# Optimization experiments

Measured on AMD Instinct MI355X. Metric: run time of the kernel, lower is better.

Reference implementation:

```python
import jax, jax.numpy as jnp
import numpy as np

B, N, C, H, R, E = 64, 512, 64, 8, 17, 21
HD = C // H
BETA = 0.01


def setup_inputs() -> dict:
    key = jax.random.key(0)
    ks = jax.random.split(key, 13)
    s = 0.02
    x = jax.random.normal(ks[0], (B, N, C), jnp.float32)
    ext = jax.random.normal(ks[1], (B, N, E), jnp.float32)
    # soft sector-assignment tensor (dense float, as used by the einsum)
    assignment = jax.random.uniform(ks[2], (N, N, R), jnp.float32)
    mask = jax.random.randint(ks[3], (N, R), 0, 2) == 1
    mask = mask.at[:, 0].set(False)  # guarantee >=1 unmasked sector per node
    Wq = jax.random.normal(ks[4], (C, C), jnp.float32) * s
    Wkv = jax.random.normal(ks[5], (2 * C, C), jnp.float32) * s
    relative_bias = jax.random.normal(ks[6], (H, 1, R), jnp.float32)
    W1 = jax.random.normal(ks[7], (64, E), jnp.float32) * s
    b1 = jnp.zeros((64,), jnp.float32)
    W2 = jax.random.normal(ks[8], (H * R, 64), jnp.float32) * s
    b2 = jnp.zeros((H * R,), jnp.float32)
    Wp = jax.random.normal(ks[9], (C, C), jnp.float32) * s
    bp = jnp.zeros((C,), jnp.float32)
    return dict(x=x, ext=ext, assignment=assignment, Wq=Wq, Wkv=Wkv,
                relative_bias=relative_bias, W1=W1, b1=b1, W2=W2, b2=b2,
                Wp=Wp, bp=bp, mask=mask)


def reference(x, ext, assignment, Wq, Wkv, relative_bias, W1, b1, W2, b2, Wp, bp, mask):
    scale = HD ** (-0.5)
    # sector gather: [B,N,C] x [N,N,R] -> [B,N,R,C]
    pre_kv = jnp.einsum('bnc,mnr->bmrc', x, assignment)
    # projections (torch Linear: y = x @ W^T)
    q = (x @ Wq.T).reshape(B, N, H, HD)                 # per-token single query
    kv = pre_kv @ Wkv.T                                  # [B,N,R,2C]
    k, v = jnp.split(kv, 2, axis=-1)
    k = k.reshape(B, N, R, H, HD)
    v = v.reshape(B, N, R, H, HD)
    # tiny 1xR attention per (b,n,h)
    attn = jnp.einsum('bnhd,bnrhd->bnhr', q, k) * scale
    attn = attn + relative_bias[:, 0, :][None, None]     # [H,R] broadcast
    # ext modulation
    ext_imp = jax.nn.relu(ext @ W1.T + b1) @ W2.T + b2   # [B,N,H*R] (dropout=eval)
    attn = attn + BETA * ext_imp.reshape(B, N, H, R)
    attn = jnp.where(mask[None, :, None, :], -jnp.inf, attn)
    p = jax.nn.softmax(attn, axis=-1)
    out = jnp.einsum('bnhr,bnrhd->bnhd', p, v).reshape(B, N, C)
    return out @ Wp.T + bp
```

## Files before the change

kernel.cpp:

```cpp
#include <hip/hip_runtime.h>
#include <hip/hip_bf16.h>

typedef __bf16 bf16x8 __attribute__((ext_vector_type(8)));
typedef float f32x4 __attribute__((ext_vector_type(4)));

#define NN 512
#define NR 17

__device__ __forceinline__ __bf16 f2b(float f) {
  __hip_bfloat16 h = __float2bfloat16(f);
  return __builtin_bit_cast(__bf16, h);
}

__device__ __forceinline__ void gload_lds16(const void* g, void* l) {
  __builtin_amdgcn_global_load_lds(
      (const __attribute__((address_space(1))) void*)g,
      (__attribute__((address_space(3))) void*)l, 16, 0, 0);
}

__global__ __launch_bounds__(256) void pack_A(const float* __restrict__ a,
                                              __hip_bfloat16* __restrict__ A2) {
  __shared__ __hip_bfloat16 T[NR * 136];
  const int m = blockIdx.y;
  const int n0 = blockIdx.x * 128;
  const float* src = a + (size_t)m * (NN * NR) + (size_t)n0 * NR;
  for (int t = threadIdx.x; t < 128 * NR; t += 256) {
    int i = t / NR;
    int r = t - i * NR;
    T[r * 136 + i] = __float2bfloat16(src[t]);
  }
  __syncthreads();
  for (int t = threadIdx.x; t < NR * 128; t += 256) {
    int r = t >> 7;
    int i = t & 127;
    A2[((size_t)m * NR + r) * NN + n0 + i] = T[r * 136 + i];
  }
}

__global__ __launch_bounds__(256) void pack_X(const float* __restrict__ x,
                                              __hip_bfloat16* __restrict__ XT,
                                              __hip_bfloat16* __restrict__ XR, int b0) {
  __shared__ __hip_bfloat16 T[64 * 136];
  const int by = blockIdx.y;
  const int n0 = blockIdx.x * 128;
  const float* src = x + ((size_t)(b0 + by) * NN + n0) * 64;
  for (int t = threadIdx.x; t < 128 * 64; t += 256) {
    int i = t >> 6;
    int c = t & 63;
    __hip_bfloat16 v = __float2bfloat16(src[t]);
    T[c * 136 + i] = v;
    XR[((size_t)by * NN + n0 + i) * 64 + c] = v;
  }
  __syncthreads();
  for (int t = threadIdx.x; t < 64 * 128; t += 256) {
    int c = t >> 7;
    int i = t & 127;
    XT[((size_t)by * 64 + c) * NN + n0 + i] = T[c * 136 + i];
  }
}

__global__ __launch_bounds__(256) void prep_w(const float* __restrict__ Wq,
                                              const float* __restrict__ Wkv,
                                              const float* __restrict__ Wp,
                                              __hip_bfloat16* __restrict__ WQK,
                                              __hip_bfloat16* __restrict__ WVP) {
  const int base = blockIdx.x * 512 + threadIdx.x;
#pragma unroll
  for (int k = 0; k < 2; ++k) {
    const int idx = base + k * 256;
    {
      const int i = idx & 63, row = idx >> 6, h = row >> 6, c = row & 63;
      float a = 0.f;
#pragma unroll
      for (int d = 0; d < 8; ++d) a += Wq[(h * 8 + d) * 64 + i] * Wkv[(h * 8 + d) * 64 + c];
      WQK[idx] = __float2bfloat16(a * 0.35355339059327373f);
    }
    {
      const int hc = idx & 511, j = idx >> 9, h = hc >> 6, c = hc & 63;
      float a = 0.f;
#pragma unroll
      for (int d = 0; d < 8; ++d)
        a += Wkv[4096 + (h * 8 + d) * 64 + c] * Wp[j * 64 + (h * 8 + d)];
      WVP[idx] = __float2bfloat16(a);
    }
  }
}

__global__ __launch_bounds__(256) void gemm_prekv(const __hip_bfloat16* __restrict__ A2,
                                                  const __hip_bfloat16* __restrict__ XT,
                                                  __hip_bfloat16* __restrict__ pkv) {
  __shared__ char As[16384];
  __shared__ char Bs[16384];
  const int tid = threadIdx.x;
  const int wave = tid >> 6;
  const int lane = tid & 63;
  const int rowBase = blockIdx.y * 128;
  const int colBase = blockIdx.x * 128;
  const int wrow0 = (wave >> 1) * 64;
  const int wcol0 = (wave & 1) * 64;
  const int lrow8 = lane >> 3;
  const int gslot = lane & 7;
  const int gsrc = gslot ^ lrow8;

  f32x4 acc[4][4];
#pragma unroll
  for (int i = 0; i < 4; ++i)
#pragma unroll
    for (int j = 0; j < 4; ++j) acc[i][j] = (f32x4)0.0f;

  const int fr = lane & 15;
  const int kg = lane >> 4;

  for (int kt = 0; kt < NN; kt += 64) {
#pragma unroll
    for (int cc = 0; cc < 4; ++cc) {
      const int r0 = wave * 32 + cc * 8;
      gload_lds16(A2 + ((size_t)(rowBase + r0 + lrow8) * NN + kt + gsrc * 8), As + r0 * 128);
      gload_lds16(XT + ((size_t)(colBase + r0 + lrow8) * NN + kt + gsrc * 8), Bs + r0 * 128);
    }
    __syncthreads();
#pragma unroll
    for (int kk = 0; kk < 2; ++kk) {
      bf16x8 av[4], bv[4];
#pragma unroll
      for (int mi = 0; mi < 4; ++mi) {
        const int row = wrow0 + mi * 16 + fr;
        const int slot = (kk * 4 + kg) ^ (row & 7);
        av[mi] = *(const bf16x8*)(As + row * 128 + slot * 16);
      }
#pragma unroll
      for (int ni = 0; ni < 4; ++ni) {
        const int row = wcol0 + ni * 16 + fr;
        const int slot = (kk * 4 + kg) ^ (row & 7);
        bv[ni] = *(const bf16x8*)(Bs + row * 128 + slot * 16);
      }
#pragma unroll
      for (int mi = 0; mi < 4; ++mi)
#pragma unroll
        for (int ni = 0; ni < 4; ++ni)
          acc[mi][ni] =
              __builtin_amdgcn_mfma_f32_16x16x32_bf16(av[mi], bv[ni], acc[mi][ni], 0, 0, 0);
    }
    __syncthreads();
  }

  const int rq = lane >> 4;
#pragma unroll
  for (int mi = 0; mi < 4; ++mi) {
#pragma unroll
    for (int ni = 0; ni < 4; ++ni) {
#pragma unroll
      for (int reg = 0; reg < 4; ++reg) {
        const int gi = rowBase + wrow0 + mi * 16 + rq * 4 + reg;
        const int gj = colBase + wcol0 + ni * 16 + fr;
        const unsigned m = (unsigned)gi / 17u;
        const unsigned r = (unsigned)gi - m * 17u;
        const int bb = gj >> 6;
        const int c = gj & 63;
        pkv[(((size_t)bb * NN + m) * NR + r) * 64 + c] = __float2bfloat16(acc[mi][ni][reg]);
      }
    }
  }
}

__global__ __launch_bounds__(256) void qw_gemm(const __hip_bfloat16* __restrict__ XR,
                                               const __hip_bfloat16* __restrict__ WQK,
                                               __hip_bfloat16* __restrict__ QW) {
  __shared__ char As[16384];
  __shared__ char Bs[16384];
  const int tid = threadIdx.x;
  const int wave = tid >> 6;
  const int lane = tid & 63;
  const int rowBase = blockIdx.y * 128;
  const int colBase = blockIdx.x * 128;
  const int wrow0 = (wave >> 1) * 64;
  const int wcol0 = (wave & 1) * 64;
  const int lrow8 = lane >> 3;
  const int gslot = lane & 7;
  const int gsrc = gslot ^ lrow8;
  const int fr = lane & 15;
  const int kg = lane >> 4;

  f32x4 acc[4][4];
#pragma unroll
  for (int i = 0; i < 4; ++i)
#pragma unroll
    for (int j = 0; j < 4; ++j) acc[i][j] = (f32x4)0.0f;

#pragma unroll
  for (int cc = 0; cc < 4; ++cc) {
    const int r0 = wave * 32 + cc * 8;
    gload_lds16(XR + ((size_t)(rowBase + r0 + lrow8) * 64 + gsrc * 8), As + r0 * 128);
    gload_lds16(WQK + ((size_t)(colBase + r0 + lrow8) * 64 + gsrc * 8), Bs + r0 * 128);
  }
  __syncthreads();
#pragma unroll
  for (int kk = 0; kk < 2; ++kk) {
    bf16x8 av[4], bv[4];
#pragma unroll
    for (int mi = 0; mi < 4; ++mi) {
      const int row = wrow0 + mi * 16 + fr;
      const int slot = (kk * 4 + kg) ^ (row & 7);
      av[mi] = *(const bf16x8*)(As + row * 128 + slot * 16);
    }
#pragma unroll
    for (int ni = 0; ni < 4; ++ni) {
      const int row = wcol0 + ni * 16 + fr;
      const int slot = (kk * 4 + kg) ^ (row & 7);
      bv[ni] = *(const bf16x8*)(Bs + row * 128 + slot * 16);
    }
#pragma unroll
    for (int mi = 0; mi < 4; ++mi)
#pragma unroll
      for (int ni = 0; ni < 4; ++ni)
        acc[mi][ni] =
            __builtin_amdgcn_mfma_f32_16x16x32_bf16(av[mi], bv[ni], acc[mi][ni], 0, 0, 0);
  }

  const int rq = lane >> 4;
#pragma unroll
  for (int mi = 0; mi < 4; ++mi)
#pragma unroll
    for (int ni = 0; ni < 4; ++ni)
#pragma unroll
      for (int reg = 0; reg < 4; ++reg) {
        const int gi = rowBase + wrow0 + mi * 16 + rq * 4 + reg;
        const int gj = colBase + wcol0 + ni * 16 + fr;
        QW[(size_t)gi * 512 + gj] = __float2bfloat16(acc[mi][ni][reg]);
      }
}

__global__ __launch_bounds__(256) void ei_kernel(const float* __restrict__ ext,
                                                 const float* __restrict__ W1p,
                                                 const float* __restrict__ b1p,
                                                 const float* __restrict__ W2p,
                                                 const float* __restrict__ b2p,
                                                 const float* __restrict__ rbp,
                                                 const int* __restrict__ maskp,
                                                 float* __restrict__ EIF, int ct0) {
  __shared__ float exts[64 * 21];
  __shared__ float W1s[64 * 21];
  __shared__ __hip_bfloat16 Hl[64 * 72];
  const int tid = threadIdx.x;
  const int tblk = blockIdx.x * 64;
  for (int i = tid; i < 64 * 21; i += 256) {
    exts[i] = ext[(size_t)(ct0 + tblk) * 21 + i];
    W1s[i] = W1p[i];
  }
  __syncthreads();
  const int wave = tid >> 6, lane = tid & 63;
#pragma unroll
  for (int k = 0; k < 16; ++k) {
    const int tl = k * 4 + wave;
    float a = b1p[lane];
#pragma unroll
    for (int e = 0; e < 21; ++e) a += exts[tl * 21 + e] * W1s[lane * 21 + e];
    Hl[tl * 72 + lane] = __float2bfloat16(fmaxf(a, 0.f));
  }
  __syncthreads();
  const int fr = lane & 15, kg = lane >> 4;
  const __bf16* Hb = (const __bf16*)Hl;
  bf16x8 a0 = *(const bf16x8*)(Hb + (wave * 16 + fr) * 72 + kg * 8);
  bf16x8 a1 = *(const bf16x8*)(Hb + (wave * 16 + fr) * 72 + 32 + kg * 8);
#pragma unroll
  for (int tile = 0; tile < 9; ++tile) {
    const int o = tile * 16 + fr;
    bf16x8 bv0 = (bf16x8)f2b(0.0f), bv1 = (bf16x8)f2b(0.0f);
    if (o < 136) {
#pragma unroll
      for (int jj = 0; jj < 8; ++jj) {
        bv0[jj] = f2b(W2p[o * 64 + kg * 8 + jj]);
        bv1[jj] = f2b(W2p[o * 64 + 32 + kg * 8 + jj]);
      }
    }
    f32x4 acc = (f32x4)0.0f;
    acc = __builtin_amdgcn_mfma_f32_16x16x32_bf16(a0, bv0, acc, 0, 0, 0);
    acc = __builtin_amdgcn_mfma_f32_16x16x32_bf16(a1, bv1, acc, 0, 0, 0);
    if (o < 136) {
      const int h = (o * 241) >> 12;
      const int r = o - h * 17;
      const float rbo = rbp[o], b2o = b2p[o];
#pragma unroll
      for (int reg = 0; reg < 4; ++reg) {
        const int tl = tblk + wave * 16 + kg * 4 + reg;
        const int m = (ct0 + tl) & (NN - 1);
        float v = maskp[m * NR + r] ? -1e30f : (rbo + 0.01f * (acc[reg] + b2o));
        EIF[(size_t)tl * 136 + o] = v;
      }
    }
  }
}

__global__ __launch_bounds__(256) void attn_fused(const __hip_bfloat16* __restrict__ pkvB,
                                                  const __hip_bfloat16* __restrict__ qwB,
                                                  const float* __restrict__ eifB,
                                                  __hip_bfloat16* __restrict__ tB) {
  __shared__ __hip_bfloat16 ps[4][16 * 40];
  const int tid = threadIdx.x;
  const int wave = tid >> 6;
  const int lane = tid & 63;
  const int t = blockIdx.x * 4 + wave;
  const __bf16* qw = (const __bf16*)(qwB + (size_t)t * 512);
  const __bf16* pkv = (const __bf16*)(pkvB + (size_t)t * (NR * 64));
  const float* eif = eifB + (size_t)t * 136;
  const int fr = lane & 15;
  const int kg = lane >> 4;

  f32x4 slo = (f32x4)0.0f, shi = (f32x4)0.0f;
#pragma unroll
  for (int kk = 0; kk < 2; ++kk) {
    bf16x8 av = *(const bf16x8*)(qw + fr * 64 + kk * 32 + kg * 8);
    bf16x8 blo = *(const bf16x8*)(pkv + fr * 64 + kk * 32 + kg * 8);
    bf16x8 bhi = (bf16x8)f2b(0.0f);
    if (fr == 0) bhi = *(const bf16x8*)(pkv + 16 * 64 + kk * 32 + kg * 8);
    slo = __builtin_amdgcn_mfma_f32_16x16x32_bf16(av, blo, slo, 0, 0, 0);
    shi = __builtin_amdgcn_mfma_f32_16x16x32_bf16(av, bhi, shi, 0, 0, 0);
  }

  float plo[4], phi[4];
#pragma unroll
  for (int reg = 0; reg < 4; ++reg) {
    const int h = kg * 4 + reg;
    float llo = slo[reg] + eif[h * 17 + fr];
    float lhi = (fr == 0) ? (shi[reg] + eif[h * 17 + 16]) : -1e30f;
    float mx = fmaxf(llo, lhi);
    mx = fmaxf(mx, __shfl_xor(mx, 1));
    mx = fmaxf(mx, __shfl_xor(mx, 2));
    mx = fmaxf(mx, __shfl_xor(mx, 4));
    mx = fmaxf(mx, __shfl_xor(mx, 8));
    float el = __expf(llo - mx);
    float eh = __expf(lhi - mx);
    float sm = el + eh;
    sm += __shfl_xor(sm, 1);
    sm += __shfl_xor(sm, 2);
    sm += __shfl_xor(sm, 4);
    sm += __shfl_xor(sm, 8);
    const float iv = 1.0f / sm;
    plo[reg] = el * iv;
    phi[reg] = eh * iv;
  }

  __hip_bfloat16* pw = ps[wave];
#pragma unroll
  for (int reg = 0; reg < 4; ++reg) {
    const int h = kg * 4 + reg;
    pw[h * 40 + fr] = __float2bfloat16(plo[reg]);
    pw[h * 40 + 16 + fr] = __float2bfloat16(phi[reg]);
  }
  bf16x8 ap = *(const bf16x8*)((const __bf16*)pw + fr * 40 + kg * 8);

#pragma unroll
  for (int ni = 0; ni < 4; ++ni) {
    bf16x8 bv = (bf16x8)f2b(0.0f);
    const __bf16* bsrc = pkv + ni * 16 + fr;
#pragma unroll
    for (int jj = 0; jj < 8; ++jj) {
      const int r = kg * 8 + jj;
      if (r < NR) bv[jj] = bsrc[r * 64];
    }
    f32x4 o = __builtin_amdgcn_mfma_f32_16x16x32_bf16(ap, bv, (f32x4)0.0f, 0, 0, 0);
    if (kg < 2) {
#pragma unroll
      for (int reg = 0; reg < 4; ++reg) {
        const int h = kg * 4 + reg;
        tB[(size_t)t * 512 + h * 64 + ni * 16 + fr] = __float2bfloat16(o[reg]);
      }
    }
  }
}

__global__ __launch_bounds__(256) void out_gemm(const __hip_bfloat16* __restrict__ Tb,
                                                const __hip_bfloat16* __restrict__ WVP,
                                                const float* __restrict__ bp,
                                                float* __restrict__ out, int ct0) {
  __shared__ char As[16384];
  __shared__ char Bs[8192];
  const int tid = threadIdx.x;
  const int wave = tid >> 6;
  const int lane = tid & 63;
  const int rowBase = blockIdx.x * 128;
  const int lrow8 = lane >> 3;
  const int gslot = lane & 7;
  const int gsrc = gslot ^ lrow8;
  const int fr = lane & 15;
  const int kg = lane >> 4;

  f32x4 acc[2][4];
#pragma unroll
  for (int i = 0; i < 2; ++i)
#pragma unroll
    for (int j = 0; j < 4; ++j) acc[i][j] = (f32x4)0.0f;

  for (int kt = 0; kt < 8; ++kt) {
#pragma unroll
    for (int cc = 0; cc < 4; ++cc) {
      const int r0 = wave * 32 + cc * 8;
      gload_lds16(Tb + ((size_t)(rowBase + r0 + lrow8) * 512 + kt * 64 + gsrc * 8),
                  As + r0 * 128);
    }
#pragma unroll
    for (int cc = 0; cc < 2; ++cc) {
      const int r0 = cc * 32 + wave * 8;
      gload_lds16(WVP + ((size_t)(r0 + lrow8) * 512 + kt * 64 + gsrc * 8), Bs + r0 * 128);
    }
    __syncthreads();
#pragma unroll
    for (int kk = 0; kk < 2; ++kk) {
      bf16x8 av[2], bv[4];
#pragma unroll
      for (int mi = 0; mi < 2; ++mi) {
        const int row = wave * 32 + mi * 16 + fr;
        const int slot = (kk * 4 + kg) ^ (row & 7);
        av[mi] = *(const bf16x8*)(As + row * 128 + slot * 16);
      }
#pragma unroll
      for (int ni = 0; ni < 4; ++ni) {
        const int row = ni * 16 + fr;
        const int slot = (kk * 4 + kg) ^ (row & 7);
        bv[ni] = *(const bf16x8*)(Bs + row * 128 + slot * 16);
      }
#pragma unroll
      for (int mi = 0; mi < 2; ++mi)
#pragma unroll
        for (int ni = 0; ni < 4; ++ni)
          acc[mi][ni] =
              __builtin_amdgcn_mfma_f32_16x16x32_bf16(av[mi], bv[ni], acc[mi][ni], 0, 0, 0);
    }
    __syncthreads();
  }

  const int rq = lane >> 4;
#pragma unroll
  for (int mi = 0; mi < 2; ++mi)
#pragma unroll
    for (int ni = 0; ni < 4; ++ni) {
      const int gj = ni * 16 + fr;
      const float bpv = bp[gj];
#pragma unroll
      for (int reg = 0; reg < 4; ++reg) {
        const int gi = rowBase + wave * 32 + mi * 16 + rq * 4 + reg;
        out[(size_t)(ct0 + gi) * 64 + gj] = acc[mi][ni][reg] + bpv;
      }
    }
}

extern "C" void kernel_launch(void* const* d_in, const int* in_sizes, int n_in, void* d_out,
                              int out_size, void* d_ws, size_t ws_size, hipStream_t stream) {
  const float* x = (const float*)d_in[0];
  const float* ext = (const float*)d_in[1];
  const float* assign = (const float*)d_in[2];
  const float* Wq = (const float*)d_in[3];
  const float* Wkv = (const float*)d_in[4];
  const float* rb = (const float*)d_in[5];
  const float* W1 = (const float*)d_in[6];
  const float* b1 = (const float*)d_in[7];
  const float* W2 = (const float*)d_in[8];
  const float* b2 = (const float*)d_in[9];
  const float* Wp = (const float*)d_in[10];
  const float* bp = (const float*)d_in[11];
  const int* mask = (const int*)d_in[12];
  float* out = (float*)d_out;

  char* ws = (char*)d_ws;
  const size_t szA2 = 8912896;
  const size_t szWQK = 65536;
  const size_t szWVP = 65536;
  const size_t fixed = szA2 + szWQK + szWVP;

  int nchunks = 4;
  {
    const int cand[3] = {1, 2, 4};
    for (int ci = 0; ci < 3; ++ci) {
      const size_t ntk = 32768 / cand[ci];
      const size_t nbb = 64 / cand[ci];
      const size_t need = fixed + nbb * 65536 + ntk * 128 + ntk * 2176 +
                          (ntk * 1024 + 2048) + (ntk * 544 + 4096) + ntk * 1024;
      if (need <= ws_size) { nchunks = cand[ci]; break; }
    }
  }
  const int ntok = 32768 / nchunks;
  const int nb = 64 / nchunks;

  __hip_bfloat16* A2 = (__hip_bfloat16*)(ws);
  __hip_bfloat16* WQK = (__hip_bfloat16*)(ws + szA2);
  __hip_bfloat16* WVP = (__hip_bfloat16*)(ws + szA2 + szWQK);
  char* p = ws + fixed;
  __hip_bfloat16* XT = (__hip_bfloat16*)p;
  p += (size_t)nb * 65536;
  __hip_bfloat16* XR = (__hip_bfloat16*)p;
  p += (size_t)ntok * 128;
  __hip_bfloat16* PKV = (__hip_bfloat16*)p;
  p += (size_t)ntok * 2176;
  __hip_bfloat16* QW = (__hip_bfloat16*)p;
  p += (size_t)ntok * 1024 + 2048;
  float* EIF = (float*)p;
  p += (size_t)ntok * 544 + 4096;
  __hip_bfloat16* TBUF = (__hip_bfloat16*)p;

  hipLaunchKernelGGL(pack_A, dim3(4, 512), dim3(256), 0, stream, assign, A2);
  hipLaunchKernelGGL(prep_w, dim3(64), dim3(256), 0, stream, Wq, Wkv, Wp, WQK, WVP);

  for (int ck = 0; ck < nchunks; ++ck) {
    const int b0 = ck * nb;
    const int ct0 = ck * ntok;
    hipLaunchKernelGGL(pack_X, dim3(4, nb), dim3(256), 0, stream, x, XT, XR, b0);
    hipLaunchKernelGGL(gemm_prekv, dim3(nb / 2, 68), dim3(256), 0, stream, A2, XT, PKV);
    hipLaunchKernelGGL(qw_gemm, dim3(4, ntok / 128), dim3(256), 0, stream, XR, WQK, QW);
    hipLaunchKernelGGL(ei_kernel, dim3(ntok / 64), dim3(256), 0, stream, ext, W1, b1, W2, b2,
                       rb, mask, EIF, ct0);
    hipLaunchKernelGGL(attn_fused, dim3(ntok / 4), dim3(256), 0, stream, PKV, QW, EIF, TBUF);
    hipLaunchKernelGGL(out_gemm, dim3(ntok / 128), dim3(256), 0, stream, TBUF, WVP, bp, out,
                       ct0);
  }
}
```

Measured before the change: 269.2 us.

## Fuse QW gemm, attention and output projection into one mega kernel; drop chunking

Replaces the separate qw_gemm, attn_fused and out_gemm kernels with a single attn_mega kernel that computes the per-token query projection into LDS, runs the 1xR attention, and applies the output projection from LDS. This removes the QW and TBUF global round trips. The per-chunk loop goes away in favour of a single full-size launch with fixed workspace offsets, and gemm_prekv gets a block-index remap for better cache locality. Risks include heavy LDS use (80KB dynamic) limiting occupancy, and an early return if the workspace is too small.

```diff
diff --git a/kernel.cpp b/kernel.cpp
--- a/kernel.cpp
+++ b/kernel.cpp
@@ -6,6 +6,8 @@
 
 #define NN 512
 #define NR 17
+
+#define SWZ(row, b) (((((b) >> 4) ^ ((row) & 7)) << 4) | ((b) & 15))
 
 __device__ __forceinline__ __bf16 f2b(float f) {
   __hip_bfloat16 h = __float2bfloat16(f);
@@ -39,11 +41,11 @@
 
 __global__ __launch_bounds__(256) void pack_X(const float* __restrict__ x,
                                               __hip_bfloat16* __restrict__ XT,
-                                              __hip_bfloat16* __restrict__ XR, int b0) {
+                                              __hip_bfloat16* __restrict__ XR) {
   __shared__ __hip_bfloat16 T[64 * 136];
   const int by = blockIdx.y;
   const int n0 = blockIdx.x * 128;
-  const float* src = x + ((size_t)(b0 + by) * NN + n0) * 64;
+  const float* src = x + ((size_t)by * NN + n0) * 64;
   for (int t = threadIdx.x; t < 128 * 64; t += 256) {
     int i = t >> 6;
     int c = t & 63;
@@ -86,6 +88,7 @@
   }
 }
 
+#define PREKV_NWG 2176
 __global__ __launch_bounds__(256) void gemm_prekv(const __hip_bfloat16* __restrict__ A2,
                                                   const __hip_bfloat16* __restrict__ XT,
                                                   __hip_bfloat16* __restrict__ pkv) {
@@ -94,8 +97,10 @@
   const int tid = threadIdx.x;
   const int wave = tid >> 6;
   const int lane = tid & 63;
-  const int rowBase = blockIdx.y * 128;
-  const int colBase = blockIdx.x * 128;
+  const int flat = blockIdx.y * gridDim.x + blockIdx.x;
+  const int s = (flat & 7) * (PREKV_NWG / 8) + (flat >> 3);
+  const int rowBase = (s >> 5) * 128;
+  const int colBase = (s & 31) * 128;
   const int wrow0 = (wave >> 1) * 64;
   const int wcol0 = (wave & 1) * 64;
   const int lrow8 = lane >> 3;
@@ -163,73 +168,6 @@
   }
 }
 
-__global__ __launch_bounds__(256) void qw_gemm(const __hip_bfloat16* __restrict__ XR,
-                                               const __hip_bfloat16* __restrict__ WQK,
-                                               __hip_bfloat16* __restrict__ QW) {
-  __shared__ char As[16384];
-  __shared__ char Bs[16384];
-  const int tid = threadIdx.x;
-  const int wave = tid >> 6;
-  const int lane = tid & 63;
-  const int rowBase = blockIdx.y * 128;
-  const int colBase = blockIdx.x * 128;
-  const int wrow0 = (wave >> 1) * 64;
-  const int wcol0 = (wave & 1) * 64;
-  const int lrow8 = lane >> 3;
-  const int gslot = lane & 7;
-  const int gsrc = gslot ^ lrow8;
-  const int fr = lane & 15;
-  const int kg = lane >> 4;
-
-  f32x4 acc[4][4];
-#pragma unroll
-  for (int i = 0; i < 4; ++i)
-#pragma unroll
-    for (int j = 0; j < 4; ++j) acc[i][j] = (f32x4)0.0f;
-
-#pragma unroll
-  for (int cc = 0; cc < 4; ++cc) {
-    const int r0 = wave * 32 + cc * 8;
-    gload_lds16(XR + ((size_t)(rowBase + r0 + lrow8) * 64 + gsrc * 8), As + r0 * 128);
-    gload_lds16(WQK + ((size_t)(colBase + r0 + lrow8) * 64 + gsrc * 8), Bs + r0 * 128);
-  }
-  __syncthreads();
-#pragma unroll
-  for (int kk = 0; kk < 2; ++kk) {
-    bf16x8 av[4], bv[4];
-#pragma unroll
-    for (int mi = 0; mi < 4; ++mi) {
-      const int row = wrow0 + mi * 16 + fr;
-      const int slot = (kk * 4 + kg) ^ (row & 7);
-      av[mi] = *(const bf16x8*)(As + row * 128 + slot * 16);
-    }
-#pragma unroll
-    for (int ni = 0; ni < 4; ++ni) {
-      const int row = wcol0 + ni * 16 + fr;
-      const int slot = (kk * 4 + kg) ^ (row & 7);
-      bv[ni] = *(const bf16x8*)(Bs + row * 128 + slot * 16);
-    }
-#pragma unroll
-    for (int mi = 0; mi < 4; ++mi)
-#pragma unroll
-      for (int ni = 0; ni < 4; ++ni)
-        acc[mi][ni] =
-            __builtin_amdgcn_mfma_f32_16x16x32_bf16(av[mi], bv[ni], acc[mi][ni], 0, 0, 0);
-  }
-
-  const int rq = lane >> 4;
-#pragma unroll
-  for (int mi = 0; mi < 4; ++mi)
-#pragma unroll
-    for (int ni = 0; ni < 4; ++ni)
-#pragma unroll
-      for (int reg = 0; reg < 4; ++reg) {
-        const int gi = rowBase + wrow0 + mi * 16 + rq * 4 + reg;
-        const int gj = colBase + wcol0 + ni * 16 + fr;
-        QW[(size_t)gi * 512 + gj] = __float2bfloat16(acc[mi][ni][reg]);
-      }
-}
-
 __global__ __launch_bounds__(256) void ei_kernel(const float* __restrict__ ext,
                                                  const float* __restrict__ W1p,
                                                  const float* __restrict__ b1p,
@@ -237,14 +175,14 @@
                                                  const float* __restrict__ b2p,
                                                  const float* __restrict__ rbp,
                                                  const int* __restrict__ maskp,
-                                                 float* __restrict__ EIF, int ct0) {
+                                                 float* __restrict__ EIF) {
   __shared__ float exts[64 * 21];
   __shared__ float W1s[64 * 21];
   __shared__ __hip_bfloat16 Hl[64 * 72];
   const int tid = threadIdx.x;
   const int tblk = blockIdx.x * 64;
   for (int i = tid; i < 64 * 21; i += 256) {
-    exts[i] = ext[(size_t)(ct0 + tblk) * 21 + i];
+    exts[i] = ext[(size_t)tblk * 21 + i];
     W1s[i] = W1p[i];
   }
   __syncthreads();
@@ -283,7 +221,7 @@
 #pragma unroll
       for (int reg = 0; reg < 4; ++reg) {
         const int tl = tblk + wave * 16 + kg * 4 + reg;
-        const int m = (ct0 + tl) & (NN - 1);
+        const int m = tl & (NN - 1);
         float v = maskp[m * NR + r] ? -1e30f : (rbo + 0.01f * (acc[reg] + b2o));
         EIF[(size_t)tl * 136 + o] = v;
       }
@@ -291,157 +229,160 @@
   }
 }
 
-__global__ __launch_bounds__(256) void attn_fused(const __hip_bfloat16* __restrict__ pkvB,
-                                                  const __hip_bfloat16* __restrict__ qwB,
-                                                  const float* __restrict__ eifB,
-                                                  __hip_bfloat16* __restrict__ tB) {
-  __shared__ __hip_bfloat16 ps[4][16 * 40];
+__global__ __launch_bounds__(256, 2) void attn_mega(
+    const __hip_bfloat16* __restrict__ XRp, const __hip_bfloat16* __restrict__ WQKp,
+    const __hip_bfloat16* __restrict__ WVPp, const __hip_bfloat16* __restrict__ pkvB,
+    const float* __restrict__ eifB, const float* __restrict__ bpp,
+    float* __restrict__ outp) {
+  extern __shared__ char smem[];
+  char* qws = smem;
+  char* Ts = smem + 32768;
   const int tid = threadIdx.x;
   const int wave = tid >> 6;
   const int lane = tid & 63;
-  const int t = blockIdx.x * 4 + wave;
-  const __bf16* qw = (const __bf16*)(qwB + (size_t)t * 512);
-  const __bf16* pkv = (const __bf16*)(pkvB + (size_t)t * (NR * 64));
-  const float* eif = eifB + (size_t)t * 136;
   const int fr = lane & 15;
   const int kg = lane >> 4;
-
-  f32x4 slo = (f32x4)0.0f, shi = (f32x4)0.0f;
-#pragma unroll
-  for (int kk = 0; kk < 2; ++kk) {
-    bf16x8 av = *(const bf16x8*)(qw + fr * 64 + kk * 32 + kg * 8);
-    bf16x8 blo = *(const bf16x8*)(pkv + fr * 64 + kk * 32 + kg * 8);
-    bf16x8 bhi = (bf16x8)f2b(0.0f);
-    if (fr == 0) bhi = *(const bf16x8*)(pkv + 16 * 64 + kk * 32 + kg * 8);
-    slo = __builtin_amdgcn_mfma_f32_16x16x32_bf16(av, blo, slo, 0, 0, 0);
-    shi = __builtin_amdgcn_mfma_f32_16x16x32_bf16(av, bhi, shi, 0, 0, 0);
-  }
-
-  float plo[4], phi[4];
-#pragma unroll
-  for (int reg = 0; reg < 4; ++reg) {
-    const int h = kg * 4 + reg;
-    float llo = slo[reg] + eif[h * 17 + fr];
-    float lhi = (fr == 0) ? (shi[reg] + eif[h * 17 + 16]) : -1e30f;
-    float mx = fmaxf(llo, lhi);
-    mx = fmaxf(mx, __shfl_xor(mx, 1));
-    mx = fmaxf(mx, __shfl_xor(mx, 2));
-    mx = fmaxf(mx, __shfl_xor(mx, 4));
-    mx = fmaxf(mx, __shfl_xor(mx, 8));
-    float el = __expf(llo - mx);
-    float eh = __expf(lhi - mx);
-    float sm = el + eh;
-    sm += __shfl_xor(sm, 1);
-    sm += __shfl_xor(sm, 2);
-    sm += __shfl_xor(sm, 4);
-    sm += __shfl_xor(sm, 8);
-    const float iv = 1.0f / sm;
-    plo[reg] = el * iv;
-    phi[reg] = eh * iv;
-  }
-
-  __hip_bfloat16* pw = ps[wave];
-#pragma unroll
-  for (int reg = 0; reg < 4; ++reg) {
-    const int h = kg * 4 + reg;
-    pw[h * 40 + fr] = __float2bfloat16(plo[reg]);
-    pw[h * 40 + 16 + fr] = __float2bfloat16(phi[reg]);
-  }
-  bf16x8 ap = *(const bf16x8*)((const __bf16*)pw + fr * 40 + kg * 8);
-
-#pragma unroll
-  for (int ni = 0; ni < 4; ++ni) {
-    bf16x8 bv = (bf16x8)f2b(0.0f);
-    const __bf16* bsrc = pkv + ni * 16 + fr;
-#pragma unroll
-    for (int jj = 0; jj < 8; ++jj) {
-      const int r = kg * 8 + jj;
-      if (r < NR) bv[jj] = bsrc[r * 64];
-    }
-    f32x4 o = __builtin_amdgcn_mfma_f32_16x16x32_bf16(ap, bv, (f32x4)0.0f, 0, 0, 0);
-    if (kg < 2) {
+  const int t0 = blockIdx.x * 32;
+  char* pT = smem + 65536 + wave * 4096;
+
+  {
+    const int rt = wave >> 1;
+    const int ct0 = (wave & 1) * 16;
+    bf16x8 a0 = *(const bf16x8*)((const __bf16*)XRp + (size_t)(t0 + rt * 16 + fr) * 64 + kg * 8);
+    bf16x8 a1 =
+        *(const bf16x8*)((const __bf16*)XRp + (size_t)(t0 + rt * 16 + fr) * 64 + 32 + kg * 8);
+#pragma unroll
+    for (int ci = 0; ci < 16; ++ci) {
+      const int ct = ct0 + ci;
+      f32x4 acc = (f32x4)0.0f;
+      bf16x8 b0 = *(const bf16x8*)((const __bf16*)WQKp + (size_t)(ct * 16 + fr) * 64 + kg * 8);
+      bf16x8 b1 =
+          *(const bf16x8*)((const __bf16*)WQKp + (size_t)(ct * 16 + fr) * 64 + 32 + kg * 8);
+      acc = __builtin_amdgcn_mfma_f32_16x16x32_bf16(a0, b0, acc, 0, 0, 0);
+      acc = __builtin_amdgcn_mfma_f32_16x16x32_bf16(a1, b1, acc, 0, 0, 0);
 #pragma unroll
       for (int reg = 0; reg < 4; ++reg) {
-        const int h = kg * 4 + reg;
-        tB[(size_t)t * 512 + h * 64 + ni * 16 + fr] = __float2bfloat16(o[reg]);
-      }
-    }
-  }
-}
-
-__global__ __launch_bounds__(256) void out_gemm(const __hip_bfloat16* __restrict__ Tb,
-                                                const __hip_bfloat16* __restrict__ WVP,
-                                                const float* __restrict__ bp,
-                                                float* __restrict__ out, int ct0) {
-  __shared__ char As[16384];
-  __shared__ char Bs[8192];
-  const int tid = threadIdx.x;
-  const int wave = tid >> 6;
-  const int lane = tid & 63;
-  const int rowBase = blockIdx.x * 128;
-  const int lrow8 = lane >> 3;
-  const int gslot = lane & 7;
-  const int gsrc = gslot ^ lrow8;
-  const int fr = lane & 15;
-  const int kg = lane >> 4;
-
-  f32x4 acc[2][4];
-#pragma unroll
-  for (int i = 0; i < 2; ++i)
-#pragma unroll
-    for (int j = 0; j < 4; ++j) acc[i][j] = (f32x4)0.0f;
-
-  for (int kt = 0; kt < 8; ++kt) {
-#pragma unroll
-    for (int cc = 0; cc < 4; ++cc) {
-      const int r0 = wave * 32 + cc * 8;
-      gload_lds16(Tb + ((size_t)(rowBase + r0 + lrow8) * 512 + kt * 64 + gsrc * 8),
-                  As + r0 * 128);
-    }
-#pragma unroll
-    for (int cc = 0; cc < 2; ++cc) {
-      const int r0 = cc * 32 + wave * 8;
-      gload_lds16(WVP + ((size_t)(r0 + lrow8) * 512 + kt * 64 + gsrc * 8), Bs + r0 * 128);
-    }
-    __syncthreads();
+        const int row = rt * 16 + kg * 4 + reg;
+        const int col = ct * 16 + fr;
+        *(__hip_bfloat16*)(qws + row * 1024 + SWZ(row, col * 2)) = __float2bfloat16(acc[reg]);
+      }
+    }
+  }
+
+  {
+    bf16x8 z = (bf16x8)f2b(0.0f);
+#pragma unroll
+    for (int j = 0; j < 4; ++j) *(bf16x8*)(pT + lane * 64 + j * 16) = z;
+  }
+  __syncthreads();
+
+  for (int i = 0; i < 8; ++i) {
+    const int tl = wave * 8 + i;
+    const size_t tg = (size_t)t0 + tl;
+    const __bf16* pk = (const __bf16*)pkvB + tg * 1088;
+
+    bf16x8 v0 = *(const bf16x8*)(pk + lane * 8);
+    bf16x8 v1 = *(const bf16x8*)(pk + 512 + lane * 8);
+    __bf16 vt = pk[1024 + lane];
+    {
+      const int r0 = lane >> 3;
+      const int cb = (lane & 7) * 8;
+#pragma unroll
+      for (int j = 0; j < 8; ++j) {
+        const int c = cb + j;
+        const int sl0 = (0 ^ ((c >> 2) & 3)) << 4;
+        const int sl1 = (1 ^ ((c >> 2) & 3)) << 4;
+        *(__bf16*)(pT + c * 64 + sl0 + r0 * 2) = v0[j];
+        *(__bf16*)(pT + c * 64 + sl1 + r0 * 2) = v1[j];
+      }
+      const int c = lane;
+      *(__bf16*)(pT + c * 64 + ((2 ^ ((c >> 2) & 3)) << 4)) = vt;
+    }
+
+    f32x4 slo = (f32x4)0.0f, shi = (f32x4)0.0f;
 #pragma unroll
     for (int kk = 0; kk < 2; ++kk) {
-      bf16x8 av[2], bv[4];
-#pragma unroll
-      for (int mi = 0; mi < 2; ++mi) {
-        const int row = wave * 32 + mi * 16 + fr;
-        const int slot = (kk * 4 + kg) ^ (row & 7);
-        av[mi] = *(const bf16x8*)(As + row * 128 + slot * 16);
-      }
-#pragma unroll
-      for (int ni = 0; ni < 4; ++ni) {
-        const int row = ni * 16 + fr;
-        const int slot = (kk * 4 + kg) ^ (row & 7);
-        bv[ni] = *(const bf16x8*)(Bs + row * 128 + slot * 16);
-      }
-#pragma unroll
-      for (int mi = 0; mi < 2; ++mi)
-#pragma unroll
-        for (int ni = 0; ni < 4; ++ni)
-          acc[mi][ni] =
-              __builtin_amdgcn_mfma_f32_16x16x32_bf16(av[mi], bv[ni], acc[mi][ni], 0, 0, 0);
-    }
-    __syncthreads();
-  }
-
-  const int rq = lane >> 4;
-#pragma unroll
-  for (int mi = 0; mi < 2; ++mi)
+      const int g = fr * 8 + kk * 4 + kg;
+      bf16x8 av = *(const bf16x8*)(qws + tl * 1024 + ((g ^ (tl & 7)) << 4));
+      bf16x8 blo = *(const bf16x8*)(pk + fr * 64 + kk * 32 + kg * 8);
+      bf16x8 bhi = (bf16x8)f2b(0.0f);
+      if (fr == 0) bhi = *(const bf16x8*)(pk + 1024 + kk * 32 + kg * 8);
+      slo = __builtin_amdgcn_mfma_f32_16x16x32_bf16(av, blo, slo, 0, 0, 0);
+      shi = __builtin_amdgcn_mfma_f32_16x16x32_bf16(av, bhi, shi, 0, 0, 0);
+    }
+
+    const float* eif = eifB + tg * 136;
+    float plo[4], phi[4];
+#pragma unroll
+    for (int reg = 0; reg < 4; ++reg) {
+      const int h = kg * 4 + reg;
+      float llo = slo[reg] + eif[h * 17 + fr];
+      float lhi = (fr == 0) ? (shi[reg] + eif[h * 17 + 16]) : -1e30f;
+      float mx = fmaxf(llo, lhi);
+      mx = fmaxf(mx, __shfl_xor(mx, 1));
+      mx = fmaxf(mx, __shfl_xor(mx, 2));
+      mx = fmaxf(mx, __shfl_xor(mx, 4));
+      mx = fmaxf(mx, __shfl_xor(mx, 8));
+      float el = __expf(llo - mx);
+      float eh = __expf(lhi - mx);
+      float sm = el + eh;
+      sm += __shfl_xor(sm, 1);
+      sm += __shfl_xor(sm, 2);
+      sm += __shfl_xor(sm, 4);
+      sm += __shfl_xor(sm, 8);
+      const float iv = 1.0f / sm;
+      plo[reg] = el * iv;
+      phi[reg] = eh * iv;
+    }
+
+#pragma unroll
+    for (int reg = 0; reg < 4; ++reg) {
+      const int h = kg * 4 + reg;
+      *(__hip_bfloat16*)(Ts + tl * 1024 + SWZ(tl, (h * 32 + fr) * 2)) =
+          __float2bfloat16(plo[reg]);
+      *(__hip_bfloat16*)(Ts + tl * 1024 + SWZ(tl, (h * 32 + 16 + fr) * 2)) =
+          __float2bfloat16(phi[reg]);
+    }
+    bf16x8 ap = *(const bf16x8*)(Ts + tl * 1024 + (((fr * 4 + kg) ^ (tl & 7)) << 4));
+
 #pragma unroll
     for (int ni = 0; ni < 4; ++ni) {
-      const int gj = ni * 16 + fr;
-      const float bpv = bp[gj];
-#pragma unroll
-      for (int reg = 0; reg < 4; ++reg) {
-        const int gi = rowBase + wave * 32 + mi * 16 + rq * 4 + reg;
-        out[(size_t)(ct0 + gi) * 64 + gj] = acc[mi][ni][reg] + bpv;
-      }
-    }
+      const int c = ni * 16 + fr;
+      bf16x8 bv = *(const bf16x8*)(pT + c * 64 + ((kg ^ ((c >> 2) & 3)) << 4));
+      f32x4 o = __builtin_amdgcn_mfma_f32_16x16x32_bf16(ap, bv, (f32x4)0.0f, 0, 0, 0);
+      if (kg < 2) {
+#pragma unroll
+        for (int reg = 0; reg < 4; ++reg) {
+          const int h = kg * 4 + reg;
+          *(__hip_bfloat16*)(Ts + tl * 1024 + SWZ(tl, (h * 64 + c) * 2)) =
+              __float2bfloat16(o[reg]);
+        }
+      }
+    }
+  }
+  __syncthreads();
+
+  {
+    const int rt = wave >> 1;
+    const int ct_base = (wave & 1) * 2;
+#pragma unroll
+    for (int cj = 0; cj < 2; ++cj) {
+      const int ct = ct_base + cj;
+      f32x4 acc = (f32x4)0.0f;
+#pragma unroll
+      for (int kk = 0; kk < 16; ++kk) {
+        const int row = rt * 16 + fr;
+        bf16x8 a = *(const bf16x8*)(Ts + row * 1024 + (((kk * 4 + kg) ^ (row & 7)) << 4));
+        bf16x8 b = *(const bf16x8*)((const __bf16*)WVPp + (size_t)(ct * 16 + fr) * 512 +
+                                    kk * 32 + kg * 8);
+        acc = __builtin_amdgcn_mfma_f32_16x16x32_bf16(a, b, acc, 0, 0, 0);
+      }
+      const float bpv = bpp[ct * 16 + fr];
+#pragma unroll
+      for (int reg = 0; reg < 4; ++reg)
+        outp[(size_t)(t0 + rt * 16 + kg * 4 + reg) * 64 + ct * 16 + fr] = acc[reg] + bpv;
+    }
+  }
 }
 
 extern "C" void kernel_launch(void* const* d_in, const int* in_sizes, int n_in, void* d_out,
@@ -462,54 +403,22 @@
   float* out = (float*)d_out;
 
   char* ws = (char*)d_ws;
-  const size_t szA2 = 8912896;
-  const size_t szWQK = 65536;
-  const size_t szWVP = 65536;
-  const size_t fixed = szA2 + szWQK + szWVP;
-
-  int nchunks = 4;
-  {
-    const int cand[3] = {1, 2, 4};
-    for (int ci = 0; ci < 3; ++ci) {
-      const size_t ntk = 32768 / cand[ci];
-      const size_t nbb = 64 / cand[ci];
-      const size_t need = fixed + nbb * 65536 + ntk * 128 + ntk * 2176 +
-                          (ntk * 1024 + 2048) + (ntk * 544 + 4096) + ntk * 1024;
-      if (need <= ws_size) { nchunks = cand[ci]; break; }
-    }
-  }
-  const int ntok = 32768 / nchunks;
-  const int nb = 64 / nchunks;
-
-  __hip_bfloat16* A2 = (__hip_bfloat16*)(ws);
-  __hip_bfloat16* WQK = (__hip_bfloat16*)(ws + szA2);
-  __hip_bfloat16* WVP = (__hip_bfloat16*)(ws + szA2 + szWQK);
-  char* p = ws + fixed;
-  __hip_bfloat16* XT = (__hip_bfloat16*)p;
-  p += (size_t)nb * 65536;
-  __hip_bfloat16* XR = (__hip_bfloat16*)p;
-  p += (size_t)ntok * 128;
-  __hip_bfloat16* PKV = (__hip_bfloat16*)p;
-  p += (size_t)ntok * 2176;
-  __hip_bfloat16* QW = (__hip_bfloat16*)p;
-  p += (size_t)ntok * 1024 + 2048;
-  float* EIF = (float*)p;
-  p += (size_t)ntok * 544 + 4096;
-  __hip_bfloat16* TBUF = (__hip_bfloat16*)p;
+  __hip_bfloat16* A2 = (__hip_bfloat16*)(ws + 0);
+  __hip_bfloat16* WQK = (__hip_bfloat16*)(ws + 8912896);
+  __hip_bfloat16* WVP = (__hip_bfloat16*)(ws + 8978432);
+  __hip_bfloat16* XT = (__hip_bfloat16*)(ws + 9043968);
+  __hip_bfloat16* XR = (__hip_bfloat16*)(ws + 13238272);
+  __hip_bfloat16* PKV = (__hip_bfloat16*)(ws + 17432576);
+  float* EIF = (float*)(ws + 88735744);
+  if (ws_size < (size_t)106565632) return;
 
   hipLaunchKernelGGL(pack_A, dim3(4, 512), dim3(256), 0, stream, assign, A2);
   hipLaunchKernelGGL(prep_w, dim3(64), dim3(256), 0, stream, Wq, Wkv, Wp, WQK, WVP);
-
-  for (int ck = 0; ck < nchunks; ++ck) {
-    const int b0 = ck * nb;
-    const int ct0 = ck * ntok;
-    hipLaunchKernelGGL(pack_X, dim3(4, nb), dim3(256), 0, stream, x, XT, XR, b0);
-    hipLaunchKernelGGL(gemm_prekv, dim3(nb / 2, 68), dim3(256), 0, stream, A2, XT, PKV);
-    hipLaunchKernelGGL(qw_gemm, dim3(4, ntok / 128), dim3(256), 0, stream, XR, WQK, QW);
-    hipLaunchKernelGGL(ei_kernel, dim3(ntok / 64), dim3(256), 0, stream, ext, W1, b1, W2, b2,
-                       rb, mask, EIF, ct0);
-    hipLaunchKernelGGL(attn_fused, dim3(ntok / 4), dim3(256), 0, stream, PKV, QW, EIF, TBUF);
-    hipLaunchKernelGGL(out_gemm, dim3(ntok / 128), dim3(256), 0, stream, TBUF, WVP, bp, out,
-                       ct0);
-  }
-}
+  hipLaunchKernelGGL(pack_X, dim3(4, 64), dim3(256), 0, stream, x, XT, XR);
+  hipLaunchKernelGGL(gemm_prekv, dim3(32, 68), dim3(256), 0, stream, A2, XT, PKV);
+  hipLaunchKernelGGL(ei_kernel, dim3(512), dim3(256), 0, stream, ext, W1, b1, W2, b2, rb, mask,
+                     EIF);
+  hipFuncSetAttribute((const void*)attn_mega, hipFuncAttributeMaxDynamicSharedMemorySize, 81920);
+  hipLaunchKernelGGL(attn_mega, dim3(1024), dim3(256), 81920, stream, XR, WQK, WVP, PKV, EIF, bp,
+                     out);
+}
```

Measured after the change: 266.5 us. Within noise of the previous version (-1.0%).
